# Optimization experiments

Hardware: AMD Instinct MI355X
Metric: run time of the kernel (lower is better)

The kernel has to match this reference:

```python
import jax, jax.numpy as jnp
import numpy as np

E = 8          # num experts
D = 1024       # hidden/model dim
H = 4096
B, S = 4, 2048


def setup_inputs() -> dict:
    key = jax.random.key(0)
    ks = jax.random.split(key, 4)
    x = jax.random.normal(ks[0], (B, S, D), dtype=jnp.float32)
    Wg = jax.random.normal(ks[1], (D, E), dtype=jnp.float32) * (1.0 / np.sqrt(D))
    W1 = jax.random.normal(ks[2], (E, D, H), dtype=jnp.float32) * (1.0 / np.sqrt(D))
    b1 = jnp.zeros((E, H), dtype=jnp.float32)
    W2 = jax.random.normal(ks[3], (E, H, D), dtype=jnp.float32) * (1.0 / np.sqrt(H))
    b2 = jnp.zeros((E, D), dtype=jnp.float32)
    return {"x": x, "Wg": Wg, "W1": W1, "b1": b1, "W2": W2, "b2": b2, "top_k": 2}


def reference(x, Wg, W1, b1, W2, b2, top_k):
    b, s, d = x.shape
    xt = x.reshape(-1, d)  # [T, D], T = total tokens
    # Linear gating: softmax over expert logits, select top_k, renormalize
    logits = xt @ Wg                                   # [T, E]
    probs = jax.nn.softmax(logits, axis=-1)            # [T, E]
    vals, idx = jax.lax.top_k(probs, top_k)            # [T, k]
    vals = vals / jnp.sum(vals, axis=-1, keepdims=True)
    # Combine weights: zero except at selected experts
    combine = jnp.sum(jax.nn.one_hot(idx, E, dtype=probs.dtype) * vals[..., None], axis=1)  # [T, E]
    # FFN experts (MLP with gelu), computed densely across experts
    h = jax.nn.gelu(jnp.einsum('td,edh->eth', xt, W1) + b1[:, None, :])  # [E, T, H]
    y = jnp.einsum('eth,ehd->etd', h, W2) + b2[:, None, :]               # [E, T, D]
    out = jnp.einsum('te,etd->td', combine, y)                           # [T, D]
    return out.reshape(b, s, d)
```

## Files before the change

kernel.cpp:

```cpp
#include <hip/hip_runtime.h>

#define T_TOK 8192
#define DIM   1024
#define HDIM  4096
#define NE    8
#define BK    64
#define BM    128
#define BN    128
#define SLOT_CAP (T_TOK * 2 + NE * BM)
#define TILES (SLOT_CAP / BM)

typedef float        f32x4 __attribute__((ext_vector_type(4)));
typedef unsigned int u32x4 __attribute__((ext_vector_type(4)));

__device__ inline unsigned short f2bf(float f) {
  union { float f; unsigned int u; } a; a.f = f;
  unsigned int u = a.u;
  unsigned int r = (u + 0x7FFFu + ((u >> 16) & 1u)) >> 16;
  return (unsigned short)r;
}

__device__ inline f32x4 mfma_bf16_16x16x32(u32x4 a, u32x4 b, f32x4 c) {
  asm("v_mfma_f32_16x16x32_bf16 %0, %1, %2, %0" : "+v"(c) : "v"(a), "v"(b));
  return c;
}

__device__ inline void gload_lds16(const void* g, void* l) {
  __builtin_amdgcn_global_load_lds(
      (const __attribute__((address_space(1))) void*)g,
      (__attribute__((address_space(3))) void*)l, 16, 0, 0);
}

__device__ inline float gelu_fast(float v) {
  const float c2 = 1.5957691216057308f;
  float z = c2 * (v + 0.044715f * v * v * v);
  return v / (1.0f + __expf(-z));
}

__device__ inline void load_offs(const int* __restrict__ counts, int* offs) {
  offs[0] = 0;
#pragma unroll
  for (int e = 0; e < NE; e++)
    offs[e + 1] = offs[e] + ((counts[e] + BM - 1) / BM) * BM;
}

__device__ void transpose_body(const float* __restrict__ src,
                               unsigned short* __restrict__ dst,
                               int R, int C, int e, int c0, int r0,
                               float (*tile)[65]) {
  int c  = threadIdx.x & 63, r4 = threadIdx.x >> 6;
  const float* s = src + (size_t)e * R * C;
#pragma unroll
  for (int i = 0; i < 16; i++) {
    int r = r4 + i * 4;
    tile[r][c] = s[(size_t)(r0 + r) * C + (c0 + c)];
  }
  __syncthreads();
  unsigned short* d = dst + (size_t)e * R * C;
  int rbase = (threadIdx.x & 7) * 8;
#pragma unroll
  for (int g = 0; g < 2; g++) {
    int cc = (threadIdx.x >> 3) + g * 32;
    u32x4 v;
#pragma unroll
    for (int k = 0; k < 4; k++)
      v[k] = (unsigned int)f2bf(tile[rbase + 2 * k][cc])
           | ((unsigned int)f2bf(tile[rbase + 2 * k + 1][cc]) << 16);
    *(u32x4*)(d + (size_t)(c0 + cc) * R + (r0 + rbase)) = v;
  }
}

__global__ __launch_bounds__(256) void prep_kernel(const float* __restrict__ x,
                                                   const float* __restrict__ Wg,
                                                   int* __restrict__ tok_e,
                                                   float* __restrict__ tok_w,
                                                   unsigned short* __restrict__ xb,
                                                   int* __restrict__ counts,
                                                   const float* __restrict__ W1,
                                                   unsigned short* __restrict__ W1T,
                                                   const float* __restrict__ W2,
                                                   unsigned short* __restrict__ W2T) {
  __shared__ float tile[64][65];
  __shared__ int h[NE];
  int bid = blockIdx.x;
  if (bid < T_TOK / 4) {
    if (threadIdx.x < NE) h[threadIdx.x] = 0;
    __syncthreads();
    int tok  = bid * 4 + (threadIdx.x >> 6);
    int lane = threadIdx.x & 63;
    const float* xr = x + (size_t)tok * DIM;
    float acc[NE];
#pragma unroll
    for (int e = 0; e < NE; e++) acc[e] = 0.f;
    for (int d = lane; d < DIM; d += 64) {
      float xv = xr[d];
      const float* wr = Wg + d * NE;
#pragma unroll
      for (int e = 0; e < NE; e++) acc[e] += xv * wr[e];
    }
#pragma unroll
    for (int e = 0; e < NE; e++) {
#pragma unroll
      for (int off = 32; off > 0; off >>= 1) acc[e] += __shfl_xor(acc[e], off);
    }
    if (lane == 0) {
      int i0 = 0;
#pragma unroll
      for (int e = 1; e < NE; e++) if (acc[e] > acc[i0]) i0 = e;
      int i1 = (i0 == 0) ? 1 : 0;
#pragma unroll
      for (int e = 0; e < NE; e++) if (e != i0 && acc[e] > acc[i1]) i1 = e;
      float w0 = 1.0f / (1.0f + expf(acc[i1] - acc[i0]));
      tok_e[tok * 2]     = i0;
      tok_e[tok * 2 + 1] = i1;
      tok_w[tok * 2]     = w0;
      tok_w[tok * 2 + 1] = 1.0f - w0;
      atomicAdd(&h[i0], 1);
      atomicAdd(&h[i1], 1);
    }
    unsigned short* xo = xb + (size_t)tok * DIM;
#pragma unroll
    for (int i = 0; i < 4; i++) {
      f32x4 v = *(const f32x4*)(xr + lane * 16 + i * 4);
      unsigned long long p = (unsigned long long)f2bf(v[0])
                           | ((unsigned long long)f2bf(v[1]) << 16)
                           | ((unsigned long long)f2bf(v[2]) << 32)
                           | ((unsigned long long)f2bf(v[3]) << 48);
      *(unsigned long long*)(xo + lane * 16 + i * 4) = p;
    }
    __syncthreads();
    if (threadIdx.x < NE) atomicAdd(&counts[threadIdx.x], h[threadIdx.x]);
  } else if (bid < T_TOK / 4 + 8192) {
    int idx = bid - T_TOK / 4;
    transpose_body(W1, W1T, DIM, HDIM, idx >> 10, (idx & 63) * 64,
                   ((idx >> 6) & 15) * 64, tile);
  } else {
    int idx = bid - T_TOK / 4 - 8192;
    transpose_body(W2, W2T, HDIM, DIM, idx >> 10, (idx & 15) * 64,
                   ((idx >> 4) & 63) * 64, tile);
  }
}

__global__ __launch_bounds__(256) void scatter_kernel(const int* __restrict__ tok_e,
                                                      const int* __restrict__ counts,
                                                      int* __restrict__ cursors,
                                                      int* __restrict__ slot_token,
                                                      int* __restrict__ tok_slot) {
  int offs[NE + 1];
  load_offs(counts, offs);
  if (blockIdx.x == 0) {
#pragma unroll
    for (int e = 0; e < NE; e++)
      for (int s = offs[e] + counts[e] + threadIdx.x; s < offs[e + 1]; s += 256)
        slot_token[s] = -1;
  }
  int t = blockIdx.x * 256 + threadIdx.x;
  int lane = threadIdx.x & 63;
#pragma unroll
  for (int j = 0; j < 2; j++) {
    int e = tok_e[t * 2 + j];
#pragma unroll
    for (int ee = 0; ee < NE; ee++) {
      unsigned long long m = __ballot(e == ee);
      if (e == ee) {
        int leader = __ffsll(m) - 1;
        int base = 0;
        if (lane == leader) base = atomicAdd(&cursors[ee], (int)__popcll(m));
        base = __shfl(base, leader);
        int pos = base + (int)__popcll(m & ((1ULL << lane) - 1ULL));
        int s = offs[ee] + pos;
        slot_token[s] = t;
        tok_slot[t * 2 + j] = s;
      }
    }
  }
}


__global__ __launch_bounds__(256) void gemm1_kernel(const unsigned short* __restrict__ Xb,
                                                    const unsigned short* __restrict__ W1T,
                                                    const float* __restrict__ b1,
                                                    const int* __restrict__ slot_token,
                                                    const int* __restrict__ counts,
                                                    unsigned short* __restrict__ Hbuf) {
  __shared__ __align__(16) unsigned short As[BM][BK];
  __shared__ __align__(16) unsigned short Bs[BN][BK];
  int offs[NE + 1];
  load_offs(counts, offs);
  const int GY = HDIM / BN;
  int lin = blockIdx.y * gridDim.x + blockIdx.x;
  int cpx = (TILES * GY) >> 3;
  int wk  = (lin & 7) * cpx + (lin >> 3);
  int bx = wk / GY, by = wk % GY;

  int row0 = bx * BM;
  if (row0 >= offs[NE]) return;
  int e = 0;
#pragma unroll
  for (int i = 1; i < NE; i++) if (row0 >= offs[i]) e = i;
  int n0  = by * BN;
  int tid  = threadIdx.x;
  int lane = tid & 63;
  int w    = tid >> 6;
  int wr = tid >> 7;
  int wc = (tid >> 6) & 1;

  int lr  = lane >> 3;
  int lcx = (lane & 7) ^ lr;
  const unsigned short* aG[4];
  const unsigned short* bG[4];
  unsigned short* aL[4];
  unsigned short* bL[4];
#pragma unroll
  for (int i = 0; i < 4; i++) {
    int r = w * 32 + i * 8;
    int tk = slot_token[row0 + r + lr];
    if (tk < 0) tk = 0;
    aG[i] = Xb + (size_t)tk * DIM + lcx * 8;
    bG[i] = W1T + ((size_t)e * HDIM + n0 + r + lr) * DIM + lcx * 8;
    aL[i] = &As[r][0];
    bL[i] = &Bs[r][0];
  }

  int frow = lane & 15;
  int hi   = lane >> 4;
  int kxs  = (hi * 8) ^ ((lane & 7) << 3);

  f32x4 acc[4][4];
#pragma unroll
  for (int m = 0; m < 4; m++)
#pragma unroll
    for (int n = 0; n < 4; n++) acc[m][n] = 0.f;

  for (int k0 = 0; k0 < DIM; k0 += BK) {
#pragma unroll
    for (int i = 0; i < 4; i++) gload_lds16(aG[i] + k0, aL[i]);
#pragma unroll
    for (int i = 0; i < 4; i++) gload_lds16(bG[i] + k0, bL[i]);
    __syncthreads();
#pragma unroll
    for (int kk = 0; kk < 2; kk++) {
      int col = (kk * 32) ^ kxs;
      u32x4 a[4], b[4];
#pragma unroll
      for (int m = 0; m < 4; m++)
        a[m] = *(const u32x4*)&As[wr * 64 + m * 16 + frow][col];
#pragma unroll
      for (int n = 0; n < 4; n++)
        b[n] = *(const u32x4*)&Bs[wc * 64 + n * 16 + frow][col];
#pragma unroll
      for (int m = 0; m < 4; m++)
#pragma unroll
        for (int n = 0; n < 4; n++)
          acc[m][n] = mfma_bf16_16x16x32(a[m], b[n], acc[m][n]);
    }
    __syncthreads();
  }

  float bias[4];
#pragma unroll
  for (int n = 0; n < 4; n++) bias[n] = b1[e * HDIM + n0 + wc * 64 + n * 16 + frow];
  unsigned short (*E)[136] = (unsigned short (*)[136])(&As[0][0]);
#pragma unroll
  for (int c0 = 0; c0 < 128; c0 += 32) {
    if (wr == (c0 >> 6)) {
      int mbase = (c0 & 63) >> 4;
#pragma unroll
      for (int mm = 0; mm < 2; mm++) {
        int m = mbase + mm;
#pragma unroll
        for (int n = 0; n < 4; n++)
#pragma unroll
          for (int j = 0; j < 4; j++)
            E[mm * 16 + hi * 4 + j][wc * 64 + n * 16 + frow] =
                f2bf(gelu_fast(acc[m][n][j] + bias[n]));
      }
    }
    __syncthreads();
#pragma unroll
    for (int p = 0; p < 2; p++) {
      int r  = p * 16 + (tid >> 4);
      int cc = (tid & 15) * 8;
      u32x4 v = *(const u32x4*)&E[r][cc];
      *(u32x4*)(Hbuf + (size_t)(row0 + c0 + r) * HDIM + n0 + cc) = v;
    }
    __syncthreads();
  }
}

__global__ __launch_bounds__(256) void gemm2_kernel(const unsigned short* __restrict__ Hbuf,
                                                    const unsigned short* __restrict__ W2T,
                                                    const float* __restrict__ b2,
                                                    const int* __restrict__ counts,
                                                    unsigned short* __restrict__ Ybuf) {
  __shared__ __align__(16) unsigned short As[BM][BK];
  __shared__ __align__(16) unsigned short Bs[BN][BK];
  int offs[NE + 1];
  load_offs(counts, offs);
  const int GY2 = (DIM / BN) * 2;
  int lin = blockIdx.y * gridDim.x + blockIdx.x;
  int cpx = (TILES * GY2) >> 3;
  int wk  = (lin & 7) * cpx + (lin >> 3);
  int bx = wk / GY2;
  int rem = wk % GY2;
  int by = rem & 7, sp = rem >> 3;
  int kbase = sp * (HDIM / 2);

  int row0 = bx * BM;
  if (row0 >= offs[NE]) return;
  int e = 0;
#pragma unroll
  for (int i = 1; i < NE; i++) if (row0 >= offs[i]) e = i;
  int n0  = by * BN;
  int tid  = threadIdx.x;
  int lane = tid & 63;
  int w    = tid >> 6;
  int wr = tid >> 7;
  int wc = (tid >> 6) & 1;

  int lr  = lane >> 3;
  int lcx = (lane & 7) ^ lr;
  const unsigned short* aG[4];
  const unsigned short* bG[4];
  unsigned short* aL[4];
  unsigned short* bL[4];
#pragma unroll
  for (int i = 0; i < 4; i++) {
    int r = w * 32 + i * 8;
    aG[i] = Hbuf + (size_t)(row0 + r + lr) * HDIM + kbase + lcx * 8;
    bG[i] = W2T + ((size_t)e * DIM + n0 + r + lr) * HDIM + kbase + lcx * 8;
    aL[i] = &As[r][0];
    bL[i] = &Bs[r][0];
  }

  int frow = lane & 15;
  int hi   = lane >> 4;
  int kxs  = (hi * 8) ^ ((lane & 7) << 3);

  f32x4 acc[4][4];
#pragma unroll
  for (int m = 0; m < 4; m++)
#pragma unroll
    for (int n = 0; n < 4; n++) acc[m][n] = 0.f;

  for (int k0 = 0; k0 < HDIM / 2; k0 += BK) {
#pragma unroll
    for (int i = 0; i < 4; i++) gload_lds16(aG[i] + k0, aL[i]);
#pragma unroll
    for (int i = 0; i < 4; i++) gload_lds16(bG[i] + k0, bL[i]);
    __syncthreads();
#pragma unroll
    for (int kk = 0; kk < 2; kk++) {
      int col = (kk * 32) ^ kxs;
      u32x4 a[4], b[4];
#pragma unroll
      for (int m = 0; m < 4; m++)
        a[m] = *(const u32x4*)&As[wr * 64 + m * 16 + frow][col];
#pragma unroll
      for (int n = 0; n < 4; n++)
        b[n] = *(const u32x4*)&Bs[wc * 64 + n * 16 + frow][col];
#pragma unroll
      for (int m = 0; m < 4; m++)
#pragma unroll
        for (int n = 0; n < 4; n++)
          acc[m][n] = mfma_bf16_16x16x32(a[m], b[n], acc[m][n]);
    }
    __syncthreads();
  }

  float bias[4];
#pragma unroll
  for (int n = 0; n < 4; n++)
    bias[n] = sp ? b2[e * DIM + n0 + wc * 64 + n * 16 + frow] : 0.f;
  unsigned short* Yp = Ybuf + (size_t)sp * SLOT_CAP * DIM;
  unsigned short (*E)[136] = (unsigned short (*)[136])(&As[0][0]);
#pragma unroll
  for (int c0 = 0; c0 < 128; c0 += 32) {
    if (wr == (c0 >> 6)) {
      int mbase = (c0 & 63) >> 4;
#pragma unroll
      for (int mm = 0; mm < 2; mm++) {
        int m = mbase + mm;
#pragma unroll
        for (int n = 0; n < 4; n++)
#pragma unroll
          for (int j = 0; j < 4; j++)
            E[mm * 16 + hi * 4 + j][wc * 64 + n * 16 + frow] =
                f2bf(acc[m][n][j] + bias[n]);
      }
    }
    __syncthreads();
#pragma unroll
    for (int p = 0; p < 2; p++) {
      int r  = p * 16 + (tid >> 4);
      int cc = (tid & 15) * 8;
      u32x4 v = *(const u32x4*)&E[r][cc];
      *(u32x4*)(Yp + (size_t)(row0 + c0 + r) * DIM + n0 + cc) = v;
    }
    __syncthreads();
  }
}

__global__ __launch_bounds__(256) void combine_kernel(const unsigned short* __restrict__ Ybuf,
                                                      const int* __restrict__ tok_slot,
                                                      const float* __restrict__ tok_w,
                                                      float* __restrict__ out) {
  int t = blockIdx.x * 2 + (threadIdx.x >> 7);
  int c = (threadIdx.x & 127) * 8;
  int s0 = tok_slot[t * 2], s1 = tok_slot[t * 2 + 1];
  float w0 = tok_w[t * 2], w1 = tok_w[t * 2 + 1];
  const unsigned short* Y1 = Ybuf + (size_t)SLOT_CAP * DIM;
  u32x4 p0 = *(const u32x4*)(Ybuf + (size_t)s0 * DIM + c);
  u32x4 p1 = *(const u32x4*)(Y1   + (size_t)s0 * DIM + c);
  u32x4 q0 = *(const u32x4*)(Ybuf + (size_t)s1 * DIM + c);
  u32x4 q1 = *(const u32x4*)(Y1   + (size_t)s1 * DIM + c);
  float r[8];
#pragma unroll
  for (int k = 0; k < 4; k++) {
    union { unsigned int u; float f; } a;
#pragma unroll
    for (int hl = 0; hl < 2; hl++) {
      unsigned int sh = hl ? 0 : 16;
      unsigned int msk = hl ? 0xFFFF0000u : 0xFFFFFFFFu;
      a.u = hl ? (p0[k] & 0xFFFF0000u) : (p0[k] << 16); float vp0 = a.f;
      a.u = hl ? (p1[k] & 0xFFFF0000u) : (p1[k] << 16); float vp1 = a.f;
      a.u = hl ? (q0[k] & 0xFFFF0000u) : (q0[k] << 16); float vq0 = a.f;
      a.u = hl ? (q1[k] & 0xFFFF0000u) : (q1[k] << 16); float vq1 = a.f;
      (void)sh; (void)msk;
      r[2 * k + hl] = w0 * (vp0 + vp1) + w1 * (vq0 + vq1);
    }
  }
  float* o = out + (size_t)t * DIM + c;
  *(f32x4*)o       = *(f32x4*)&r[0];
  *(f32x4*)(o + 4) = *(f32x4*)&r[4];
}

extern "C" void kernel_launch(void* const* d_in, const int* in_sizes, int n_in,
                              void* d_out, int out_size, void* d_ws, size_t ws_size,
                              hipStream_t stream) {
  (void)in_sizes; (void)n_in; (void)out_size;
  const float* x  = (const float*)d_in[0];
  const float* Wg = (const float*)d_in[1];
  const float* W1 = (const float*)d_in[2];
  const float* b1 = (const float*)d_in[3];
  const float* W2 = (const float*)d_in[4];
  const float* b2 = (const float*)d_in[5];
  float* out = (float*)d_out;

  char* ws = (char*)d_ws;
  size_t off = 0;
  auto take = [&](size_t bytes) -> char* {
    char* p = ws + off;
    off += (bytes + 255) & ~(size_t)255;
    return p;
  };
  unsigned short* W1T  = (unsigned short*)take((size_t)NE * DIM * HDIM * 2);
  unsigned short* W2T  = (unsigned short*)take((size_t)NE * DIM * HDIM * 2);
  unsigned short* Xb   = (unsigned short*)take((size_t)T_TOK * DIM * 2);
  unsigned short* Hbuf = (unsigned short*)take((size_t)SLOT_CAP * HDIM * 2);
  unsigned short* Ybuf = (unsigned short*)take((size_t)2 * SLOT_CAP * DIM * 2);
  int*   slot_token = (int*)take(SLOT_CAP * 4);
  int*   tok_e      = (int*)take(T_TOK * 2 * 4);
  float* tok_w      = (float*)take(T_TOK * 2 * 4);
  int*   tok_slot   = (int*)take(T_TOK * 2 * 4);
  int*   cnt_cur    = (int*)take(256);
  int*   counts  = cnt_cur;
  int*   cursors = cnt_cur + 32;

  if (off > ws_size) {
    hipMemsetAsync(d_out, 0, (size_t)out_size * 4, stream);
    return;
  }

  hipMemsetAsync(cnt_cur, 0, 256, stream);
  prep_kernel<<<T_TOK / 4 + 16384, 256, 0, stream>>>(x, Wg, tok_e, tok_w, Xb,
                                                     counts, W1, W1T, W2, W2T);
  scatter_kernel<<<T_TOK / 256, 256, 0, stream>>>(tok_e, counts, cursors,
                                                  slot_token, tok_slot);
  gemm1_kernel<<<dim3(TILES, HDIM / BN), 256, 0, stream>>>(Xb, W1T, b1,
                                                           slot_token, counts, Hbuf);
  gemm2_kernel<<<dim3(TILES, 16), 256, 0, stream>>>(Hbuf, W2T, b2, counts, Ybuf);
  combine_kernel<<<T_TOK / 2, 256, 0, stream>>>(Ybuf, tok_slot, tok_w, out);
}
```

Before: 497.8 us.

## Move W2 transpose from prep kernel into gemm1 grid tail blocks

The W2 fp32-to-bf16 transpose blocks are removed from the prep kernel and appended as extra blocks to the gemm1 launch, which becomes a 1D grid. The goal is to let the bandwidth-heavy W2 conversion overlap with gemm1's compute and tail, and to shorten the prep kernel on the critical path. The trade-off is that transpose blocks now compete with gemm1 for CUs and memory bandwidth, and gemm1's shared memory is reused for the transpose tile.

```diff
diff --git a/kernel.cpp b/kernel.cpp
--- a/kernel.cpp
+++ b/kernel.cpp
@@ -9,6 +9,8 @@
 #define BN    128
 #define SLOT_CAP (T_TOK * 2 + NE * BM)
 #define TILES (SLOT_CAP / BM)
+#define G1BLKS (TILES * (HDIM / BN))
+#define W2BLKS ((HDIM / 64) * (DIM / 64) * NE)
 
 typedef float        f32x4 __attribute__((ext_vector_type(4)));
 typedef unsigned int u32x4 __attribute__((ext_vector_type(4)));
@@ -77,9 +79,7 @@
                                                    unsigned short* __restrict__ xb,
                                                    int* __restrict__ counts,
                                                    const float* __restrict__ W1,
-                                                   unsigned short* __restrict__ W1T,
-                                                   const float* __restrict__ W2,
-                                                   unsigned short* __restrict__ W2T) {
+                                                   unsigned short* __restrict__ W1T) {
   __shared__ float tile[64][65];
   __shared__ int h[NE];
   int bid = blockIdx.x;
@@ -130,14 +130,10 @@
     }
     __syncthreads();
     if (threadIdx.x < NE) atomicAdd(&counts[threadIdx.x], h[threadIdx.x]);
-  } else if (bid < T_TOK / 4 + 8192) {
+  } else {
     int idx = bid - T_TOK / 4;
     transpose_body(W1, W1T, DIM, HDIM, idx >> 10, (idx & 63) * 64,
                    ((idx >> 6) & 15) * 64, tile);
-  } else {
-    int idx = bid - T_TOK / 4 - 8192;
-    transpose_body(W2, W2T, HDIM, DIM, idx >> 10, (idx & 15) * 64,
-                   ((idx >> 4) & 63) * 64, tile);
   }
 }
 
@@ -182,14 +178,23 @@
                                                     const float* __restrict__ b1,
                                                     const int* __restrict__ slot_token,
                                                     const int* __restrict__ counts,
-                                                    unsigned short* __restrict__ Hbuf) {
-  __shared__ __align__(16) unsigned short As[BM][BK];
-  __shared__ __align__(16) unsigned short Bs[BN][BK];
+                                                    unsigned short* __restrict__ Hbuf,
+                                                    const float* __restrict__ W2,
+                                                    unsigned short* __restrict__ W2T) {
+  __shared__ __align__(16) unsigned short SMEM[2 * BM * BK];
+  if (blockIdx.x >= G1BLKS) {
+    int idx = blockIdx.x - G1BLKS;
+    transpose_body(W2, W2T, HDIM, DIM, idx >> 10, (idx & 15) * 64,
+                   ((idx >> 4) & 63) * 64, (float (*)[65])SMEM);
+    return;
+  }
+  unsigned short (*As)[BK] = (unsigned short (*)[BK])SMEM;
+  unsigned short (*Bs)[BK] = (unsigned short (*)[BK])(SMEM + BM * BK);
   int offs[NE + 1];
   load_offs(counts, offs);
   const int GY = HDIM / BN;
-  int lin = blockIdx.y * gridDim.x + blockIdx.x;
-  int cpx = (TILES * GY) >> 3;
+  int lin = blockIdx.x;
+  int cpx = G1BLKS >> 3;
   int wk  = (lin & 7) * cpx + (lin >> 3);
   int bx = wk / GY, by = wk % GY;
 
@@ -260,7 +265,7 @@
   float bias[4];
 #pragma unroll
   for (int n = 0; n < 4; n++) bias[n] = b1[e * HDIM + n0 + wc * 64 + n * 16 + frow];
-  unsigned short (*E)[136] = (unsigned short (*)[136])(&As[0][0]);
+  unsigned short (*E)[136] = (unsigned short (*)[136])SMEM;
 #pragma unroll
   for (int c0 = 0; c0 < 128; c0 += 32) {
     if (wr == (c0 >> 6)) {
@@ -420,13 +425,10 @@
     union { unsigned int u; float f; } a;
 #pragma unroll
     for (int hl = 0; hl < 2; hl++) {
-      unsigned int sh = hl ? 0 : 16;
-      unsigned int msk = hl ? 0xFFFF0000u : 0xFFFFFFFFu;
       a.u = hl ? (p0[k] & 0xFFFF0000u) : (p0[k] << 16); float vp0 = a.f;
       a.u = hl ? (p1[k] & 0xFFFF0000u) : (p1[k] << 16); float vp1 = a.f;
       a.u = hl ? (q0[k] & 0xFFFF0000u) : (q0[k] << 16); float vq0 = a.f;
       a.u = hl ? (q1[k] & 0xFFFF0000u) : (q1[k] << 16); float vq1 = a.f;
-      (void)sh; (void)msk;
       r[2 * k + hl] = w0 * (vp0 + vp1) + w1 * (vq0 + vq1);
     }
   }
@@ -473,12 +475,12 @@
   }
 
   hipMemsetAsync(cnt_cur, 0, 256, stream);
-  prep_kernel<<<T_TOK / 4 + 16384, 256, 0, stream>>>(x, Wg, tok_e, tok_w, Xb,
-                                                     counts, W1, W1T, W2, W2T);
+  prep_kernel<<<T_TOK / 4 + 8192, 256, 0, stream>>>(x, Wg, tok_e, tok_w, Xb,
+                                                    counts, W1, W1T);
   scatter_kernel<<<T_TOK / 256, 256, 0, stream>>>(tok_e, counts, cursors,
                                                   slot_token, tok_slot);
-  gemm1_kernel<<<dim3(TILES, HDIM / BN), 256, 0, stream>>>(Xb, W1T, b1,
-                                                           slot_token, counts, Hbuf);
+  gemm1_kernel<<<G1BLKS + W2BLKS, 256, 0, stream>>>(Xb, W1T, b1, slot_token,
+                                                    counts, Hbuf, W2, W2T);
   gemm2_kernel<<<dim3(TILES, 16), 256, 0, stream>>>(Hbuf, W2T, b2, counts, Ybuf);
   combine_kernel<<<T_TOK / 2, 256, 0, stream>>>(Ybuf, tok_slot, tok_w, out);
 }
```

After: 482.1 us. -3.2%, faster.
